# Kernel tuning notes

Measured on AMD Instinct MI355X. Metric: run time of the kernel, lower is better.

## Reference

```python
import jax, jax.numpy as jnp
import numpy as np

N = 50000      # nodes
E = 800000     # edges (avg degree 16)
IN = 128       # input feature dim
HID = 32       # per-head hidden dim
OUT = 64       # per-head output dim
H = 2          # heads per layer
NEG = 0.2      # leaky relu negative slope


def setup_inputs() -> dict:
    key = jax.random.key(0)
    ks = jax.random.split(key, 16)
    x = jax.random.normal(ks[0], (N, IN), dtype=jnp.float32)
    src = jax.random.randint(ks[1], (E,), 0, N)
    dst = jax.random.randint(ks[2], (E,), 0, N)

    def lin(k, fin, fout):
        return jax.random.normal(k, (fin, fout), dtype=jnp.float32) * (1.0 / np.sqrt(fin))

    def attn(k, h, d):
        return jax.random.normal(k, (h, d), dtype=jnp.float32) * 0.1

    # layer 0: IN -> H*HID, layer 1: H*HID -> H*HID, layer 2 (output): H*HID -> H*OUT
    W0, al0, ar0, b0 = lin(ks[3], IN, H * HID), attn(ks[4], H, HID), attn(ks[5], H, HID), jnp.zeros((H * HID,), jnp.float32)
    W1, al1, ar1, b1 = lin(ks[6], H * HID, H * HID), attn(ks[7], H, HID), attn(ks[8], H, HID), jnp.zeros((H * HID,), jnp.float32)
    W2, al2, ar2, b2 = lin(ks[9], H * HID, H * OUT), attn(ks[10], H, OUT), attn(ks[11], H, OUT), jnp.zeros((H * OUT,), jnp.float32)
    return {"x": x, "src": src, "dst": dst,
            "W0": W0, "al0": al0, "ar0": ar0, "b0": b0,
            "W1": W1, "al1": al1, "ar1": ar1, "b1": b1,
            "W2": W2, "al2": al2, "ar2": ar2, "b2": b2}


def gat_conv(x, src, dst, W, al, ar, b, heads, out_dim, apply_relu):
    # feat: [N, H, D]
    feat = (x @ W).reshape(-1, heads, out_dim)
    el = jnp.einsum('nhd,hd->nh', feat, al)   # [N, H]
    er = jnp.einsum('nhd,hd->nh', feat, ar)   # [N, H]
    # per-edge attention logits, leaky-relu
    e = jax.nn.leaky_relu(el[src] + er[dst], NEG)          # [E, H]
    # edge softmax over incoming edges of each dst node (numerically stable)
    m = jax.ops.segment_max(e, dst, num_segments=N)        # [N, H]
    m = jnp.where(jnp.isfinite(m), m, 0.0)                 # nodes w/o in-edges
    ex = jnp.exp(e - m[dst])                               # [E, H]
    s = jax.ops.segment_sum(ex, dst, num_segments=N)       # [N, H]
    alpha = ex / s[dst]                                    # [E, H]
    # weighted aggregate of source features into dst nodes
    rst = jax.ops.segment_sum(feat[src] * alpha[:, :, None], dst, num_segments=N)  # [N, H, D]
    rst = rst + b.reshape(1, heads, out_dim)
    if apply_relu:
        rst = jax.nn.relu(rst)
    return rst


def reference(x, src, dst, W0, al0, ar0, b0, W1, al1, ar1, b1, W2, al2, ar2, b2):
    h = gat_conv(x, src, dst, W0, al0, ar0, b0, H, HID, True).reshape(N, H * HID)   # flatten(1)
    h = gat_conv(h, src, dst, W1, al1, ar1, b1, H, HID, True).reshape(N, H * HID)   # flatten(1)
    logits = gat_conv(h, src, dst, W2, al2, ar2, b2, H, OUT, False).mean(axis=1)    # mean over heads -> [N, OUT]
    return logits
```

## Files before the change

kernel.cpp:

```cpp
#include <hip/hip_runtime.h>
#include <hip/hip_bf16.h>
#include <hip/hip_fp16.h>

#define NNODES 50000
#define NEG_SLOPE 0.2f
#define BKT_SHIFT 8
#define NBKT ((NNODES + 255) >> 8)
#define STRIDE 5120
#define PCHUNK 2048
#define PEPT 8

typedef _Float16 half8 __attribute__((ext_vector_type(8)));
typedef float v4f __attribute__((ext_vector_type(4)));

__device__ __forceinline__ int rfl(int v) { return __builtin_amdgcn_readfirstlane(v); }

__device__ __forceinline__ void pack_one(const float* W, _Float16* Wp, int K, int C, int tid) {
    int KC = K / 32;
    int l = tid & 63;
    int kc = (tid >> 6) % KC;
    int t = tid / (KC * 64);
    int cc = l & 15, q = l >> 4;
    half8 b;
#pragma unroll
    for (int j = 0; j < 8; j++)
        b[j] = (_Float16)W[(size_t)(kc * 32 + q * 8 + j) * C + t * 16 + cc];
    *(half8*)(Wp + (size_t)tid * 8) = b;
}

__global__ __launch_bounds__(256) void kernelAB(
    const float* __restrict__ x, const float* __restrict__ W0,
    const float* __restrict__ AL, const float* __restrict__ AR,
    _Float16* __restrict__ featA, float2* __restrict__ el2A, float2* __restrict__ er2A,
    const float* __restrict__ W2, _Float16* __restrict__ Wp2,
    const int* __restrict__ src, const int* __restrict__ dst,
    int* __restrict__ bcursor, int2* __restrict__ ebuf, int E, int N) {
    int blk = blockIdx.x;
    if (blk >= 786) {
        __shared__ int hist[NBKT];
        __shared__ int gbase[NBKT];
        int t = threadIdx.x;
        for (int i = t; i < NBKT; i += 256) hist[i] = 0;
        __syncthreads();
        int base = (blk - 786) * PCHUNK;
        int sreg[PEPT], dreg[PEPT], rreg[PEPT], breg[PEPT];
#pragma unroll
        for (int k = 0; k < PEPT; k++) {
            int i = base + k * 256 + t;
            if (i < E) {
                sreg[k] = src[i];
                dreg[k] = dst[i];
                breg[k] = dreg[k] >> BKT_SHIFT;
                rreg[k] = atomicAdd(&hist[breg[k]], 1);
            } else {
                breg[k] = -1;
            }
        }
        __syncthreads();
        for (int i = t; i < NBKT; i += 256)
            if (hist[i]) gbase[i] = i * STRIDE + atomicAdd(&bcursor[i * 16], hist[i]);
        __syncthreads();
#pragma unroll
        for (int k = 0; k < PEPT; k++) {
            if (breg[k] >= 0)
                ebuf[(size_t)(gbase[breg[k]] + rreg[k])] = make_int2(sreg[k], dreg[k]);
        }
        return;
    }
    if (blk >= 782) {
        int tid = (blk - 782) * 256 + threadIdx.x;
        if (tid < 8 * 2 * 64) pack_one(W2, Wp2, 64, 128, tid);
        return;
    }
    int wave = threadIdx.x >> 6, lane = threadIdx.x & 63;
    int mtile = blk * 4 + wave;
    if (mtile * 16 >= N) return;
    int m0 = mtile * 16;
    int c = lane & 15, q = lane >> 4;
    v4f acc[4];
#pragma unroll
    for (int t = 0; t < 4; t++) acc[t] = (v4f){0.f, 0.f, 0.f, 0.f};
    const size_t arow = (size_t)(m0 + c) * 128 + q * 8;
#pragma unroll
    for (int kc = 0; kc < 4; kc++) {
        const float* xr = x + arow + kc * 32;
        float4 f0 = *(const float4*)xr;
        float4 f1 = *(const float4*)(xr + 4);
        float fv[8] = {f0.x, f0.y, f0.z, f0.w, f1.x, f1.y, f1.z, f1.w};
        half8 ah, av;
#pragma unroll
        for (int j = 0; j < 8; j++) {
            ah[j] = (_Float16)fv[j];
            av[j] = (_Float16)(fv[j] - (float)ah[j]);
        }
#pragma unroll
        for (int tt = 0; tt < 4; tt++) {
            half8 b;
#pragma unroll
            for (int j = 0; j < 8; j++)
                b[j] = (_Float16)W0[(size_t)(kc * 32 + q * 8 + j) * 64 + tt * 16 + c];
            acc[tt] = __builtin_amdgcn_mfma_f32_16x16x32_f16(ah, b, acc[tt], 0, 0, 0);
            acc[tt] = __builtin_amdgcn_mfma_f32_16x16x32_f16(av, b, acc[tt], 0, 0, 0);
        }
    }
#pragma unroll
    for (int tt = 0; tt < 4; tt++)
#pragma unroll
        for (int r = 0; r < 4; r++) {
            int row = m0 + q * 4 + r;
            featA[(size_t)row * 64 + tt * 16 + c] = (_Float16)acc[tt][r];
        }
    float alv[4], arv[4];
#pragma unroll
    for (int tt = 0; tt < 4; tt++) { alv[tt] = AL[tt * 16 + c]; arv[tt] = AR[tt * 16 + c]; }
#pragma unroll
    for (int r = 0; r < 4; r++) {
        float l0 = 0.f, l1 = 0.f, r0 = 0.f, r1 = 0.f;
#pragma unroll
        for (int tt = 0; tt < 4; tt++) {
            float v = acc[tt][r];
            if (tt < 2) { l0 = fmaf(v, alv[tt], l0); r0 = fmaf(v, arv[tt], r0); }
            else        { l1 = fmaf(v, alv[tt], l1); r1 = fmaf(v, arv[tt], r1); }
        }
#pragma unroll
        for (int m = 1; m < 16; m <<= 1) {
            l0 += __shfl_xor(l0, m, 64);
            l1 += __shfl_xor(l1, m, 64);
            r0 += __shfl_xor(r0, m, 64);
            r1 += __shfl_xor(r1, m, 64);
        }
        if (c == 0) {
            int row = m0 + q * 4 + r;
            el2A[row] = make_float2(l0, l1);
            er2A[row] = make_float2(r0, r1);
        }
    }
}

__global__ __launch_bounds__(1024) void local_sort(const int2* __restrict__ ebuf,
                                                   const int* __restrict__ bcursor,
                                                   int2* __restrict__ rowse,
                                                   int* __restrict__ csrc, int N) {
    __shared__ int lcnt[256], lrow[256], ws[4];
    int b = blockIdx.x;
    int d0 = b << BKT_SHIFT;
    int t = threadIdx.x;
    int base = b * STRIDE;
    int endE = base + bcursor[b * 16];
    if (t < 256) lcnt[t] = 0;
    __syncthreads();
    for (int i = base + t; i < endE; i += 1024)
        atomicAdd(&lcnt[ebuf[i].y - d0], 1);
    __syncthreads();
    int v = (t < 256) ? lcnt[t] : 0;
    int lane = t & 63;
    int x = v;
#pragma unroll
    for (int m = 1; m < 64; m <<= 1) {
        int y = __shfl_up(x, m, 64);
        if (lane >= m) x += y;
    }
    if (t < 256 && lane == 63) ws[t >> 6] = x;
    __syncthreads();
    if (t < 256) {
        int w = t >> 6, waveoff = 0;
#pragma unroll
        for (int k = 0; k < 4; k++) if (k < w) waveoff += ws[k];
        int excl = base + waveoff + x - v;
        lrow[t] = excl;
        int d = d0 + t;
        if (d < N) rowse[d] = make_int2(excl, excl + v);
        lcnt[t] = 0;
    }
    __syncthreads();
    for (int i = base + t; i < endE; i += 1024) {
        int2 e = ebuf[i];
        int ld = e.y - d0;
        int p = lrow[ld] + atomicAdd(&lcnt[ld], 1);
        csrc[p] = e.x;
    }
}

__global__ __launch_bounds__(256) void agg0_gemm1(
    const int2* __restrict__ rowse, const int* __restrict__ csrc,
    const float2* __restrict__ el2A, const float2* __restrict__ er2A,
    const _Float16* __restrict__ featA, const float* __restrict__ b0,
    const float* __restrict__ W1, const float* __restrict__ al1, const float* __restrict__ ar1,
    _Float16* __restrict__ featB, float2* __restrict__ el2B, float2* __restrict__ er2B,
    int N) {
    __shared__ __attribute__((aligned(16))) int   stS[4][64];
    __shared__ __attribute__((aligned(16))) float stX[4][64], stY[4][64];
    __shared__ float vbuf[4][64];
    __shared__ float4 w1v[16 * 64];
    int wave = threadIdx.x >> 6, lane = threadIdx.x & 63, h = lane >> 5;
    for (int i = threadIdx.x; i < 64 * 64; i += 256) {
        int k = i >> 6, cc = i & 63;
        ((float*)w1v)[((((k >> 2) << 6) + cc) << 2) | (k & 3)] = W1[i];
    }
    __syncthreads();
    float bl = b0[lane];
    float al1v = al1[lane], ar1v = ar1[lane];
    const int*   stSw = stS[wave];
    const float* stWH = h ? stY[wave] : stX[wave];
    for (int n0 = blockIdx.x * 4 + wave; n0 < N; n0 += gridDim.x * 4) {
        int n = rfl(n0);
        int2 se = rowse[n];
        int beg = rfl(se.x), end = rfl(se.y);
        float2 rr = er2A[n];
        float s = 0.f, acc = 0.f;
        for (int base = beg; base < end; base += 64) {
            int idx = base + lane;
            bool act = idx < end;
            int sv = act ? csrc[idx] : 0;
            stS[wave][lane] = sv;
            float wxv = 0.f, wyv = 0.f;
            if (act) {
                float2 l = el2A[sv];
                float t0 = l.x + rr.x; t0 = t0 > 0.f ? t0 : NEG_SLOPE * t0;
                float t1 = l.y + rr.y; t1 = t1 > 0.f ? t1 : NEG_SLOPE * t1;
                wxv = __expf(t0); wyv = __expf(t1);
            }
            stX[wave][lane] = wxv;
            stY[wave][lane] = wyv;
            int cnt = (min(64, end - base) + 7) & ~7;
            for (int j = 0; j < cnt; j += 8) {
                int4 sA = *(const int4*)(stSw + j);
                int4 sB = *(const int4*)(stSw + j + 4);
                float f0 = (float)featA[(size_t)sA.x * 64 + lane];
                float f1 = (float)featA[(size_t)sA.y * 64 + lane];
                float f2 = (float)featA[(size_t)sA.z * 64 + lane];
                float f3 = (float)featA[(size_t)sA.w * 64 + lane];
                float f4 = (float)featA[(size_t)sB.x * 64 + lane];
                float f5 = (float)featA[(size_t)sB.y * 64 + lane];
                float f6 = (float)featA[(size_t)sB.z * 64 + lane];
                float f7 = (float)featA[(size_t)sB.w * 64 + lane];
                float4 wv0 = *(const float4*)(stWH + j);
                float4 wv1 = *(const float4*)(stWH + j + 4);
                s += ((wv0.x + wv0.y) + (wv0.z + wv0.w)) + ((wv1.x + wv1.y) + (wv1.z + wv1.w));
                acc = fmaf(wv0.x, f0, acc);
                acc = fmaf(wv0.y, f1, acc);
                acc = fmaf(wv0.z, f2, acc);
                acc = fmaf(wv0.w, f3, acc);
                acc = fmaf(wv1.x, f4, acc);
                acc = fmaf(wv1.y, f5, acc);
                acc = fmaf(wv1.z, f6, acc);
                acc = fmaf(wv1.w, f7, acc);
            }
        }
        float v = (s > 0.f) ? acc / s : 0.f;
        v = fmaxf(v + bl, 0.f);
        vbuf[wave][lane] = v;
        const float4* vv = (const float4*)vbuf[wave];
        float f = 0.f;
#pragma unroll
        for (int kk = 0; kk < 16; kk++) {
            float4 v4 = vv[kk];
            float4 w4 = w1v[(kk << 6) + lane];
            f = fmaf(v4.x, w4.x, f);
            f = fmaf(v4.y, w4.y, f);
            f = fmaf(v4.z, w4.z, f);
            f = fmaf(v4.w, w4.w, f);
        }
        featB[(size_t)n * 64 + lane] = (_Float16)f;
        float vl = f * al1v, vr = f * ar1v;
#pragma unroll
        for (int m = 1; m < 32; m <<= 1) {
            vl += __shfl_xor(vl, m, 64);
            vr += __shfl_xor(vr, m, 64);
        }
        if ((lane & 31) == 0) {
            ((float*)el2B)[n * 2 + h] = vl;
            ((float*)er2B)[n * 2 + h] = vr;
        }
    }
}

__global__ __launch_bounds__(256) void aggregate32(
    const int2* __restrict__ rowse, const int* __restrict__ csrc,
    const float2* __restrict__ el2, const float2* __restrict__ er2,
    const _Float16* __restrict__ feat16, const float* __restrict__ b,
    _Float16* __restrict__ ahi, _Float16* __restrict__ alo, int N) {
    __shared__ __attribute__((aligned(16))) int   stS0[4][64], stS1[4][64];
    __shared__ __attribute__((aligned(16))) float stX0[4][64], stY0[4][64];
    __shared__ __attribute__((aligned(16))) float stX1[4][64], stY1[4][64];
    int wave = threadIdx.x >> 6, lane = threadIdx.x & 63, h = lane >> 5;
    int g = rfl(blockIdx.x * 4 + wave);
    int n0 = 2 * g, n1 = n0 + 1;
    if (n0 >= N) return;
    bool has1 = (n1 < N);
    float bl = b[lane];
    int2 se0 = rowse[n0];
    int2 se1 = has1 ? rowse[n1] : make_int2(0, 0);
    int beg0 = rfl(se0.x), len0 = rfl(se0.y) - beg0;
    int beg1 = rfl(se1.x), len1 = rfl(se1.y) - beg1;
    float2 rr0 = er2[n0];
    float2 rr1 = has1 ? er2[n1] : make_float2(0.f, 0.f);
    const int*   stSw0 = stS0[wave];
    const int*   stSw1 = stS1[wave];
    const float* stWH0 = h ? stY0[wave] : stX0[wave];
    const float* stWH1 = h ? stY1[wave] : stX1[wave];
    float s0 = 0.f, acc0 = 0.f, s1 = 0.f, acc1 = 0.f;
    int chunks = max(len0, len1);
    for (int off = 0; off < chunks; off += 64) {
        bool a0 = off + lane < len0;
        bool a1 = off + lane < len1;
        int sv0 = a0 ? csrc[beg0 + off + lane] : 0;
        int sv1 = a1 ? csrc[beg1 + off + lane] : 0;
        stS0[wave][lane] = sv0;
        stS1[wave][lane] = sv1;
        float wx0 = 0.f, wy0 = 0.f, wx1 = 0.f, wy1 = 0.f;
        if (a0) {
            float2 l = el2[sv0];
            float t0 = l.x + rr0.x; t0 = t0 > 0.f ? t0 : NEG_SLOPE * t0;
            float t1 = l.y + rr0.y; t1 = t1 > 0.f ? t1 : NEG_SLOPE * t1;
            wx0 = __expf(t0); wy0 = __expf(t1);
        }
        if (a1) {
            float2 l = el2[sv1];
            float t0 = l.x + rr1.x; t0 = t0 > 0.f ? t0 : NEG_SLOPE * t0;
            float t1 = l.y + rr1.y; t1 = t1 > 0.f ? t1 : NEG_SLOPE * t1;
            wx1 = __expf(t0); wy1 = __expf(t1);
        }
        stX0[wave][lane] = wx0; stY0[wave][lane] = wy0;
        stX1[wave][lane] = wx1; stY1[wave][lane] = wy1;
        int cnt = (min(64, chunks - off) + 7) & ~7;
        for (int j = 0; j < cnt; j += 8) {
            int4 sA = *(const int4*)(stSw0 + j);
            int4 sB = *(const int4*)(stSw0 + j + 4);
            int4 tA = *(const int4*)(stSw1 + j);
            int4 tB = *(const int4*)(stSw1 + j + 4);
            float f0 = (float)feat16[(size_t)sA.x * 64 + lane];
            float f1 = (float)feat16[(size_t)sA.y * 64 + lane];
            float f2 = (float)feat16[(size_t)sA.z * 64 + lane];
            float f3 = (float)feat16[(size_t)sA.w * 64 + lane];
            float f4 = (float)feat16[(size_t)sB.x * 64 + lane];
            float f5 = (float)feat16[(size_t)sB.y * 64 + lane];
            float f6 = (float)feat16[(size_t)sB.z * 64 + lane];
            float f7 = (float)feat16[(size_t)sB.w * 64 + lane];
            float p0 = (float)feat16[(size_t)tA.x * 64 + lane];
            float p1 = (float)feat16[(size_t)tA.y * 64 + lane];
            float p2 = (float)feat16[(size_t)tA.z * 64 + lane];
            float p3 = (float)feat16[(size_t)tA.w * 64 + lane];
            float p4 = (float)feat16[(size_t)tB.x * 64 + lane];
            float p5 = (float)feat16[(size_t)tB.y * 64 + lane];
            float p6 = (float)feat16[(size_t)tB.z * 64 + lane];
            float p7 = (float)feat16[(size_t)tB.w * 64 + lane];
            float4 wv0 = *(const float4*)(stWH0 + j);
            float4 wv1 = *(const float4*)(stWH0 + j + 4);
            float4 xv0 = *(const float4*)(stWH1 + j);
            float4 xv1 = *(const float4*)(stWH1 + j + 4);
            s0 += ((wv0.x + wv0.y) + (wv0.z + wv0.w)) + ((wv1.x + wv1.y) + (wv1.z + wv1.w));
            acc0 = fmaf(wv0.x, f0, acc0);
            acc0 = fmaf(wv0.y, f1, acc0);
            acc0 = fmaf(wv0.z, f2, acc0);
            acc0 = fmaf(wv0.w, f3, acc0);
            acc0 = fmaf(wv1.x, f4, acc0);
            acc0 = fmaf(wv1.y, f5, acc0);
            acc0 = fmaf(wv1.z, f6, acc0);
            acc0 = fmaf(wv1.w, f7, acc0);
            s1 += ((xv0.x + xv0.y) + (xv0.z + xv0.w)) + ((xv1.x + xv1.y) + (xv1.z + xv1.w));
            acc1 = fmaf(xv0.x, p0, acc1);
            acc1 = fmaf(xv0.y, p1, acc1);
            acc1 = fmaf(xv0.z, p2, acc1);
            acc1 = fmaf(xv0.w, p3, acc1);
            acc1 = fmaf(xv1.x, p4, acc1);
            acc1 = fmaf(xv1.y, p5, acc1);
            acc1 = fmaf(xv1.z, p6, acc1);
            acc1 = fmaf(xv1.w, p7, acc1);
        }
    }
    float v = (s0 > 0.f) ? acc0 / s0 : 0.f;
    v = fmaxf(v + bl, 0.f);
    _Float16 hv = (_Float16)v;
    ahi[(size_t)n0 * 64 + lane] = hv;
    alo[(size_t)n0 * 64 + lane] = (_Float16)(v - (float)hv);
    if (has1) {
        float u = (s1 > 0.f) ? acc1 / s1 : 0.f;
        u = fmaxf(u + bl, 0.f);
        _Float16 hu = (_Float16)u;
        ahi[(size_t)n1 * 64 + lane] = hu;
        alo[(size_t)n1 * 64 + lane] = (_Float16)(u - (float)hu);
    }
}

__global__ __launch_bounds__(256) void gemm_mfma2(
    const _Float16* __restrict__ Ahi, const _Float16* __restrict__ Alo,
    const _Float16* __restrict__ Wp,
    const float* __restrict__ AL, const float* __restrict__ AR,
    __half2* __restrict__ feat2, float2* __restrict__ el2, float2* __restrict__ er2,
    int N) {
    constexpr int KC = 2, NT = 8;
    int wave = threadIdx.x >> 6, lane = threadIdx.x & 63;
    int mtile = blockIdx.x * 4 + wave;
    if (mtile * 16 >= N) return;
    int m0 = mtile * 16;
    int c = lane & 15, q = lane >> 4;
    v4f acc[NT];
#pragma unroll
    for (int t = 0; t < NT; t++) acc[t] = (v4f){0.f, 0.f, 0.f, 0.f};
    const size_t arow = (size_t)(m0 + c) * 64 + q * 8;
#pragma unroll
    for (int kc = 0; kc < KC; kc++) {
        half8 ah = *(const half8*)(Ahi + arow + kc * 32);
        half8 av = *(const half8*)(Alo + arow + kc * 32);
#pragma unroll
        for (int t = 0; t < NT; t++) {
            half8 b = *(const half8*)(Wp + ((size_t)(t * KC + kc) * 64 + lane) * 8);
            acc[t] = __builtin_amdgcn_mfma_f32_16x16x32_f16(ah, b, acc[t], 0, 0, 0);
            acc[t] = __builtin_amdgcn_mfma_f32_16x16x32_f16(av, b, acc[t], 0, 0, 0);
        }
    }
#pragma unroll
    for (int t = 0; t < NT / 2; t++)
#pragma unroll
        for (int r = 0; r < 4; r++) {
            int row = m0 + q * 4 + r;
            feat2[(size_t)row * 64 + t * 16 + c] =
                __floats2half2_rn(acc[t][r], acc[t + NT / 2][r]);
        }
    float alv[NT], arv[NT];
#pragma unroll
    for (int t = 0; t < NT; t++) { alv[t] = AL[t * 16 + c]; arv[t] = AR[t * 16 + c]; }
#pragma unroll
    for (int r = 0; r < 4; r++) {
        float l0 = 0.f, l1 = 0.f, r0 = 0.f, r1 = 0.f;
#pragma unroll
        for (int t = 0; t < NT; t++) {
            float v = acc[t][r];
            if (t < NT / 2) { l0 = fmaf(v, alv[t], l0); r0 = fmaf(v, arv[t], r0); }
            else            { l1 = fmaf(v, alv[t], l1); r1 = fmaf(v, arv[t], r1); }
        }
#pragma unroll
        for (int m = 1; m < 16; m <<= 1) {
            l0 += __shfl_xor(l0, m, 64);
            l1 += __shfl_xor(l1, m, 64);
            r0 += __shfl_xor(r0, m, 64);
            r1 += __shfl_xor(r1, m, 64);
        }
        if (c == 0) {
            int row = m0 + q * 4 + r;
            el2[row] = make_float2(l0, l1);
            er2[row] = make_float2(r0, r1);
        }
    }
}

__global__ __launch_bounds__(256) void aggregate64_mean(
    const int2* __restrict__ rowse, const int* __restrict__ csrc,
    const float2* __restrict__ el2, const float2* __restrict__ er2,
    const __half2* __restrict__ feat2, const float* __restrict__ b,
    float* __restrict__ out, int N) {
    __shared__ __attribute__((aligned(16))) int   stS0[4][64], stS1[4][64];
    __shared__ __attribute__((aligned(16))) float stX0[4][64], stY0[4][64];
    __shared__ __attribute__((aligned(16))) float stX1[4][64], stY1[4][64];
    int wave = threadIdx.x >> 6, lane = threadIdx.x & 63;
    int g = rfl(blockIdx.x * 4 + wave);
    int n0 = 2 * g, n1 = n0 + 1;
    if (n0 >= N) return;
    bool has1 = (n1 < N);
    float b0v = b[lane], b1v = b[64 + lane];
    int2 se0 = rowse[n0];
    int2 se1 = has1 ? rowse[n1] : make_int2(0, 0);
    int beg0 = rfl(se0.x), len0 = rfl(se0.y) - beg0;
    int beg1 = rfl(se1.x), len1 = rfl(se1.y) - beg1;
    float2 rr0 = er2[n0];
    float2 rr1 = has1 ? er2[n1] : make_float2(0.f, 0.f);
    const int* stSw0 = stS0[wave];
    const int* stSw1 = stS1[wave];
    float s00 = 0.f, s01 = 0.f, a00 = 0.f, a01 = 0.f;
    float s10 = 0.f, s11 = 0.f, a10 = 0.f, a11 = 0.f;
    int chunks = max(len0, len1);
    for (int off = 0; off < chunks; off += 64) {
        bool a0 = off + lane < len0;
        bool a1 = off + lane < len1;
        int sv0 = a0 ? csrc[beg0 + off + lane] : 0;
        int sv1 = a1 ? csrc[beg1 + off + lane] : 0;
        stS0[wave][lane] = sv0;
        stS1[wave][lane] = sv1;
        float wx0 = 0.f, wy0 = 0.f, wx1 = 0.f, wy1 = 0.f;
        if (a0) {
            float2 l = el2[sv0];
            float t0 = l.x + rr0.x; t0 = t0 > 0.f ? t0 : NEG_SLOPE * t0;
            float t1 = l.y + rr0.y; t1 = t1 > 0.f ? t1 : NEG_SLOPE * t1;
            wx0 = __expf(t0); wy0 = __expf(t1);
        }
        if (a1) {
            float2 l = el2[sv1];
            float t0 = l.x + rr1.x; t0 = t0 > 0.f ? t0 : NEG_SLOPE * t0;
            float t1 = l.y + rr1.y; t1 = t1 > 0.f ? t1 : NEG_SLOPE * t1;
            wx1 = __expf(t0); wy1 = __expf(t1);
        }
        stX0[wave][lane] = wx0; stY0[wave][lane] = wy0;
        stX1[wave][lane] = wx1; stY1[wave][lane] = wy1;
        int cnt = (min(64, chunks - off) + 7) & ~7;
        for (int j = 0; j < cnt; j += 8) {
            int4 sA = *(const int4*)(stSw0 + j);
            int4 sB = *(const int4*)(stSw0 + j + 4);
            int4 tA = *(const int4*)(stSw1 + j);
            int4 tB = *(const int4*)(stSw1 + j + 4);
            float2 fv0[8], fv1[8];
            fv0[0] = __half22float2(feat2[(size_t)sA.x * 64 + lane]);
            fv0[1] = __half22float2(feat2[(size_t)sA.y * 64 + lane]);
            fv0[2] = __half22float2(feat2[(size_t)sA.z * 64 + lane]);
            fv0[3] = __half22float2(feat2[(size_t)sA.w * 64 + lane]);
            fv0[4] = __half22float2(feat2[(size_t)sB.x * 64 + lane]);
            fv0[5] = __half22float2(feat2[(size_t)sB.y * 64 + lane]);
            fv0[6] = __half22float2(feat2[(size_t)sB.z * 64 + lane]);
            fv0[7] = __half22float2(feat2[(size_t)sB.w * 64 + lane]);
            fv1[0] = __half22float2(feat2[(size_t)tA.x * 64 + lane]);
            fv1[1] = __half22float2(feat2[(size_t)tA.y * 64 + lane]);
            fv1[2] = __half22float2(feat2[(size_t)tA.z * 64 + lane]);
            fv1[3] = __half22float2(feat2[(size_t)tA.w * 64 + lane]);
            fv1[4] = __half22float2(feat2[(size_t)tB.x * 64 + lane]);
            fv1[5] = __half22float2(feat2[(size_t)tB.y * 64 + lane]);
            fv1[6] = __half22float2(feat2[(size_t)tB.z * 64 + lane]);
            fv1[7] = __half22float2(feat2[(size_t)tB.w * 64 + lane]);
            float4 wx0v = *(const float4*)(stX0[wave] + j);
            float4 wx0w = *(const float4*)(stX0[wave] + j + 4);
            float4 wy0v = *(const float4*)(stY0[wave] + j);
            float4 wy0w = *(const float4*)(stY0[wave] + j + 4);
            float4 wx1v = *(const float4*)(stX1[wave] + j);
            float4 wx1w = *(const float4*)(stX1[wave] + j + 4);
            float4 wy1v = *(const float4*)(stY1[wave] + j);
            float4 wy1w = *(const float4*)(stY1[wave] + j + 4);
            float wxs0[8] = {wx0v.x, wx0v.y, wx0v.z, wx0v.w, wx0w.x, wx0w.y, wx0w.z, wx0w.w};
            float wys0[8] = {wy0v.x, wy0v.y, wy0v.z, wy0v.w, wy0w.x, wy0w.y, wy0w.z, wy0w.w};
            float wxs1[8] = {wx1v.x, wx1v.y, wx1v.z, wx1v.w, wx1w.x, wx1w.y, wx1w.z, wx1w.w};
            float wys1[8] = {wy1v.x, wy1v.y, wy1v.z, wy1v.w, wy1w.x, wy1w.y, wy1w.z, wy1w.w};
#pragma unroll
            for (int u = 0; u < 8; u++) {
                s00 += wxs0[u]; s01 += wys0[u];
                a00 = fmaf(wxs0[u], fv0[u].x, a00);
                a01 = fmaf(wys0[u], fv0[u].y, a01);
            }
#pragma unroll
            for (int u = 0; u < 8; u++) {
                s10 += wxs1[u]; s11 += wys1[u];
                a10 = fmaf(wxs1[u], fv1[u].x, a10);
                a11 = fmaf(wys1[u], fv1[u].y, a11);
            }
        }
    }
    float v0 = (s00 > 0.f) ? a00 / s00 : 0.f;
    float v1 = (s01 > 0.f) ? a01 / s01 : 0.f;
    out[(size_t)n0 * 64 + lane] = 0.5f * ((v0 + b0v) + (v1 + b1v));
    if (has1) {
        float u0 = (s10 > 0.f) ? a10 / s10 : 0.f;
        float u1 = (s11 > 0.f) ? a11 / s11 : 0.f;
        out[(size_t)n1 * 64 + lane] = 0.5f * ((u0 + b0v) + (u1 + b1v));
    }
}


extern "C" void kernel_launch(void* const* d_in, const int* in_sizes, int n_in,
                              void* d_out, int out_size, void* d_ws, size_t ws_size,
                              hipStream_t stream) {
    const float* x   = (const float*)d_in[0];
    const int*   src = (const int*)d_in[1];
    const int*   dst = (const int*)d_in[2];
    const float* W0  = (const float*)d_in[3];
    const float* al0 = (const float*)d_in[4];
    const float* ar0 = (const float*)d_in[5];
    const float* b0  = (const float*)d_in[6];
    const float* W1  = (const float*)d_in[7];
    const float* al1 = (const float*)d_in[8];
    const float* ar1 = (const float*)d_in[9];
    const float* b1  = (const float*)d_in[10];
    const float* W2  = (const float*)d_in[11];
    const float* al2 = (const float*)d_in[12];
    const float* ar2 = (const float*)d_in[13];
    const float* b2  = (const float*)d_in[14];
    float* out = (float*)d_out;

    const int N = NNODES;
    const int E = in_sizes[1];

    char* p = (char*)d_ws;
    auto alloc = [&](size_t bytes) {
        void* r = (void*)p;
        p += (bytes + 255) & ~(size_t)255;
        return r;
    };
    int*    bcursor = (int*)alloc((size_t)NBKT * 16 * 4);
    int2*   rowse   = (int2*)alloc((size_t)N * 8);
    int2*   ebuf    = (int2*)alloc(((size_t)NBKT * STRIDE + 4096) * 8);
    int*    csrc    = (int*)alloc(((size_t)NBKT * STRIDE + 4096) * 4);
    float2* el2A    = (float2*)alloc((size_t)N * 8);
    float2* er2A    = (float2*)alloc((size_t)N * 8);
    float2* el2B    = (float2*)alloc((size_t)N * 8);
    float2* er2B    = (float2*)alloc((size_t)N * 8);
    _Float16* ahi   = (_Float16*)alloc((size_t)N * 64 * 2);
    _Float16* alo   = (_Float16*)alloc((size_t)N * 64 * 2);
    void*   featA   = alloc((size_t)N * 64 * 4);
    _Float16* featB = (_Float16*)alloc((size_t)N * 64 * 2);
    _Float16* Wp2   = (_Float16*)alloc(8 * 2 * 64 * 8 * 2);

    hipMemsetAsync(bcursor, 0, (size_t)NBKT * 16 * 4, stream);
    int nch = (E + PCHUNK - 1) / PCHUNK;
    kernelAB<<<786 + nch, 256, 0, stream>>>(x, W0, al0, ar0, (_Float16*)featA, el2A, er2A,
                                            W2, Wp2, src, dst, bcursor, ebuf, E, N);
    local_sort<<<NBKT, 1024, 0, stream>>>(ebuf, bcursor, rowse, csrc, N);

    agg0_gemm1<<<2048, 256, 0, stream>>>(rowse, csrc, el2A, er2A, (const _Float16*)featA,
                                         b0, W1, al1, ar1, featB, el2B, er2B, N);
    int npair = (N + 1) / 2;
    int nbp = (npair + 3) / 4;
    aggregate32<<<nbp, 256, 0, stream>>>(rowse, csrc, el2B, er2B, featB, b1, ahi, alo, N);
    int gb = (N / 16 + 3) / 4;
    gemm_mfma2<<<gb, 256, 0, stream>>>(ahi, alo, Wp2, al2, ar2, (__half2*)featA, el2A, er2A, N);
    aggregate64_mean<<<nbp, 256, 0, stream>>>(rowse, csrc, el2A, er2A, (const __half2*)featA,
                                              b2, out, N);
}
```

Measured before the change: 225.0 us.

## Regroup launches: partition with weight packing, then co-schedule local sort with GEMM0

```diff
diff --git a/kernel.cpp b/kernel.cpp
--- a/kernel.cpp
+++ b/kernel.cpp
@@ -28,52 +28,101 @@
     *(half8*)(Wp + (size_t)tid * 8) = b;
 }
 
-__global__ __launch_bounds__(256) void kernelAB(
-    const float* __restrict__ x, const float* __restrict__ W0,
+__global__ __launch_bounds__(256) void kernelP(
+    const int* __restrict__ src, const int* __restrict__ dst,
+    int* __restrict__ bcursor, int2* __restrict__ ebuf,
+    const float* __restrict__ W0, _Float16* __restrict__ Wp0,
+    const float* __restrict__ W2, _Float16* __restrict__ Wp2,
+    int E, int nch) {
+    int blk = blockIdx.x;
+    if (blk >= nch + 4) {
+        int tid = (blk - nch - 4) * 256 + threadIdx.x;
+        if (tid < 8 * 2 * 64) pack_one(W2, Wp2, 64, 128, tid);
+        return;
+    }
+    if (blk >= nch) {
+        int tid = (blk - nch) * 256 + threadIdx.x;
+        if (tid < 4 * 4 * 64) pack_one(W0, Wp0, 128, 64, tid);
+        return;
+    }
+    __shared__ int hist[NBKT];
+    __shared__ int gbase[NBKT];
+    int t = threadIdx.x;
+    for (int i = t; i < NBKT; i += 256) hist[i] = 0;
+    __syncthreads();
+    int base = blk * PCHUNK;
+    int sreg[PEPT], dreg[PEPT], rreg[PEPT], breg[PEPT];
+#pragma unroll
+    for (int k = 0; k < PEPT; k++) {
+        int i = base + k * 256 + t;
+        if (i < E) {
+            sreg[k] = src[i];
+            dreg[k] = dst[i];
+            breg[k] = dreg[k] >> BKT_SHIFT;
+            rreg[k] = atomicAdd(&hist[breg[k]], 1);
+        } else {
+            breg[k] = -1;
+        }
+    }
+    __syncthreads();
+    for (int i = t; i < NBKT; i += 256)
+        if (hist[i]) gbase[i] = i * STRIDE + atomicAdd(&bcursor[i * 16], hist[i]);
+    __syncthreads();
+#pragma unroll
+    for (int k = 0; k < PEPT; k++) {
+        if (breg[k] >= 0)
+            ebuf[(size_t)(gbase[breg[k]] + rreg[k])] = make_int2(sreg[k], dreg[k]);
+    }
+}
+
+__global__ __launch_bounds__(256) void kernelAB2(
+    const float* __restrict__ x, const _Float16* __restrict__ Wp0,
     const float* __restrict__ AL, const float* __restrict__ AR,
     _Float16* __restrict__ featA, float2* __restrict__ el2A, float2* __restrict__ er2A,
-    const float* __restrict__ W2, _Float16* __restrict__ Wp2,
-    const int* __restrict__ src, const int* __restrict__ dst,
-    int* __restrict__ bcursor, int2* __restrict__ ebuf, int E, int N) {
+    const int2* __restrict__ ebuf, const int* __restrict__ bcursor,
+    int2* __restrict__ rowse, int* __restrict__ csrc, int N) {
     int blk = blockIdx.x;
-    if (blk >= 786) {
-        __shared__ int hist[NBKT];
-        __shared__ int gbase[NBKT];
+    if (blk < NBKT) {
+        __shared__ int lcnt[256], lrow[256], ws[4];
+        int b = blk;
+        int d0 = b << BKT_SHIFT;
         int t = threadIdx.x;
-        for (int i = t; i < NBKT; i += 256) hist[i] = 0;
+        int base = b * STRIDE;
+        int endE = base + bcursor[b * 16];
+        lcnt[t] = 0;
         __syncthreads();
-        int base = (blk - 786) * PCHUNK;
-        int sreg[PEPT], dreg[PEPT], rreg[PEPT], breg[PEPT];
-#pragma unroll
-        for (int k = 0; k < PEPT; k++) {
-            int i = base + k * 256 + t;
-            if (i < E) {
-                sreg[k] = src[i];
-                dreg[k] = dst[i];
-                breg[k] = dreg[k] >> BKT_SHIFT;
-                rreg[k] = atomicAdd(&hist[breg[k]], 1);
-            } else {
-                breg[k] = -1;
-            }
-        }
+        for (int i = base + t; i < endE; i += 256)
+            atomicAdd(&lcnt[ebuf[i].y - d0], 1);
         __syncthreads();
-        for (int i = t; i < NBKT; i += 256)
-            if (hist[i]) gbase[i] = i * STRIDE + atomicAdd(&bcursor[i * 16], hist[i]);
+        int v = lcnt[t];
+        int lane = t & 63;
+        int xx = v;
+#pragma unroll
+        for (int m = 1; m < 64; m <<= 1) {
+            int y = __shfl_up(xx, m, 64);
+            if (lane >= m) xx += y;
+        }
+        if (lane == 63) ws[t >> 6] = xx;
         __syncthreads();
-#pragma unroll
-        for (int k = 0; k < PEPT; k++) {
-            if (breg[k] >= 0)
-                ebuf[(size_t)(gbase[breg[k]] + rreg[k])] = make_int2(sreg[k], dreg[k]);
+        int w = t >> 6, waveoff = 0;
+#pragma unroll
+        for (int k = 0; k < 4; k++) if (k < w) waveoff += ws[k];
+        int excl = base + waveoff + xx - v;
+        lrow[t] = excl;
+        int d = d0 + t;
+        if (d < N) rowse[d] = make_int2(excl, excl + v);
+        lcnt[t] = 0;
+        __syncthreads();
+        for (int i = base + t; i < endE; i += 256) {
+            int2 e = ebuf[i];
+            int ld = e.y - d0;
+            int p = lrow[ld] + atomicAdd(&lcnt[ld], 1);
+            csrc[p] = e.x;
         }
         return;
     }
-    if (blk >= 782) {
-        int tid = (blk - 782) * 256 + threadIdx.x;
-        if (tid < 8 * 2 * 64) pack_one(W2, Wp2, 64, 128, tid);
-        return;
-    }
     int wave = threadIdx.x >> 6, lane = threadIdx.x & 63;
-    int mtile = blk * 4 + wave;
+    int mtile = (blk - NBKT) * 4 + wave;
     if (mtile * 16 >= N) return;
     int m0 = mtile * 16;
     int c = lane & 15, q = lane >> 4;
@@ -95,10 +144,7 @@
         }
 #pragma unroll
         for (int tt = 0; tt < 4; tt++) {
-            half8 b;
-#pragma unroll
-            for (int j = 0; j < 8; j++)
-                b[j] = (_Float16)W0[(size_t)(kc * 32 + q * 8 + j) * 64 + tt * 16 + c];
+            half8 b = *(const half8*)(Wp0 + ((size_t)(tt * 4 + kc) * 64 + lane) * 8);
             acc[tt] = __builtin_amdgcn_mfma_f32_16x16x32_f16(ah, b, acc[tt], 0, 0, 0);
             acc[tt] = __builtin_amdgcn_mfma_f32_16x16x32_f16(av, b, acc[tt], 0, 0, 0);
         }
@@ -134,50 +180,6 @@
             el2A[row] = make_float2(l0, l1);
             er2A[row] = make_float2(r0, r1);
         }
-    }
-}
-
-__global__ __launch_bounds__(1024) void local_sort(const int2* __restrict__ ebuf,
-                                                   const int* __restrict__ bcursor,
-                                                   int2* __restrict__ rowse,
-                                                   int* __restrict__ csrc, int N) {
-    __shared__ int lcnt[256], lrow[256], ws[4];
-    int b = blockIdx.x;
-    int d0 = b << BKT_SHIFT;
-    int t = threadIdx.x;
-    int base = b * STRIDE;
-    int endE = base + bcursor[b * 16];
-    if (t < 256) lcnt[t] = 0;
-    __syncthreads();
-    for (int i = base + t; i < endE; i += 1024)
-        atomicAdd(&lcnt[ebuf[i].y - d0], 1);
-    __syncthreads();
-    int v = (t < 256) ? lcnt[t] : 0;
-    int lane = t & 63;
-    int x = v;
-#pragma unroll
-    for (int m = 1; m < 64; m <<= 1) {
-        int y = __shfl_up(x, m, 64);
-        if (lane >= m) x += y;
-    }
-    if (t < 256 && lane == 63) ws[t >> 6] = x;
-    __syncthreads();
-    if (t < 256) {
-        int w = t >> 6, waveoff = 0;
-#pragma unroll
-        for (int k = 0; k < 4; k++) if (k < w) waveoff += ws[k];
-        int excl = base + waveoff + x - v;
-        lrow[t] = excl;
-        int d = d0 + t;
-        if (d < N) rowse[d] = make_int2(excl, excl + v);
-        lcnt[t] = 0;
-    }
-    __syncthreads();
-    for (int i = base + t; i < endE; i += 1024) {
-        int2 e = ebuf[i];
-        int ld = e.y - d0;
-        int p = lrow[ld] + atomicAdd(&lcnt[ld], 1);
-        csrc[p] = e.x;
     }
 }
 
@@ -594,13 +596,13 @@
     void*   featA   = alloc((size_t)N * 64 * 4);
     _Float16* featB = (_Float16*)alloc((size_t)N * 64 * 2);
     _Float16* Wp2   = (_Float16*)alloc(8 * 2 * 64 * 8 * 2);
+    _Float16* Wp0   = (_Float16*)alloc(4 * 4 * 64 * 8 * 2);
 
     hipMemsetAsync(bcursor, 0, (size_t)NBKT * 16 * 4, stream);
     int nch = (E + PCHUNK - 1) / PCHUNK;
-    kernelAB<<<786 + nch, 256, 0, stream>>>(x, W0, al0, ar0, (_Float16*)featA, el2A, er2A,
-                                            W2, Wp2, src, dst, bcursor, ebuf, E, N);
-    local_sort<<<NBKT, 1024, 0, stream>>>(ebuf, bcursor, rowse, csrc, N);
-
+    kernelP<<<nch + 8, 256, 0, stream>>>(src, dst, bcursor, ebuf, W0, Wp0, W2, Wp2, E, nch);
+    kernelAB2<<<NBKT + 782, 256, 0, stream>>>(x, Wp0, al0, ar0, (_Float16*)featA, el2A, er2A,
+                                              ebuf, bcursor, rowse, csrc, N);
     agg0_gemm1<<<2048, 256, 0, stream>>>(rowse, csrc, el2A, er2A, (const _Float16*)featA,
                                          b0, W1, al1, ar1, featB, el2B, er2B, N);
     int npair = (N + 1) / 2;
```

New measurement: 230.6 us. 2.5% more time.

## Split layer-1 fused aggregate+FMA GEMM into aggregate32 plus MFMA GEMM kernel

Applied to the files above, without the earlier changes.

```diff
diff --git a/kernel.cpp b/kernel.cpp
--- a/kernel.cpp
+++ b/kernel.cpp
@@ -33,16 +33,17 @@
     const float* __restrict__ AL, const float* __restrict__ AR,
     _Float16* __restrict__ featA, float2* __restrict__ el2A, float2* __restrict__ er2A,
     const float* __restrict__ W2, _Float16* __restrict__ Wp2,
+    const float* __restrict__ W1, _Float16* __restrict__ Wp1,
     const int* __restrict__ src, const int* __restrict__ dst,
     int* __restrict__ bcursor, int2* __restrict__ ebuf, int E, int N) {
     int blk = blockIdx.x;
-    if (blk >= 786) {
+    if (blk >= 788) {
         __shared__ int hist[NBKT];
         __shared__ int gbase[NBKT];
         int t = threadIdx.x;
         for (int i = t; i < NBKT; i += 256) hist[i] = 0;
         __syncthreads();
-        int base = (blk - 786) * PCHUNK;
+        int base = (blk - 788) * PCHUNK;
         int sreg[PEPT], dreg[PEPT], rreg[PEPT], breg[PEPT];
 #pragma unroll
         for (int k = 0; k < PEPT; k++) {
@@ -65,6 +66,11 @@
             if (breg[k] >= 0)
                 ebuf[(size_t)(gbase[breg[k]] + rreg[k])] = make_int2(sreg[k], dreg[k]);
         }
+        return;
+    }
+    if (blk >= 786) {
+        int tid = (blk - 786) * 256 + threadIdx.x;
+        if (tid < 4 * 2 * 64) pack_one(W1, Wp1, 64, 64, tid);
         return;
     }
     if (blk >= 782) {
@@ -178,100 +184,6 @@
         int ld = e.y - d0;
         int p = lrow[ld] + atomicAdd(&lcnt[ld], 1);
         csrc[p] = e.x;
-    }
-}
-
-__global__ __launch_bounds__(256) void agg0_gemm1(
-    const int2* __restrict__ rowse, const int* __restrict__ csrc,
-    const float2* __restrict__ el2A, const float2* __restrict__ er2A,
-    const _Float16* __restrict__ featA, const float* __restrict__ b0,
-    const float* __restrict__ W1, const float* __restrict__ al1, const float* __restrict__ ar1,
-    _Float16* __restrict__ featB, float2* __restrict__ el2B, float2* __restrict__ er2B,
-    int N) {
-    __shared__ __attribute__((aligned(16))) int   stS[4][64];
-    __shared__ __attribute__((aligned(16))) float stX[4][64], stY[4][64];
-    __shared__ float vbuf[4][64];
-    __shared__ float4 w1v[16 * 64];
-    int wave = threadIdx.x >> 6, lane = threadIdx.x & 63, h = lane >> 5;
-    for (int i = threadIdx.x; i < 64 * 64; i += 256) {
-        int k = i >> 6, cc = i & 63;
-        ((float*)w1v)[((((k >> 2) << 6) + cc) << 2) | (k & 3)] = W1[i];
-    }
-    __syncthreads();
-    float bl = b0[lane];
-    float al1v = al1[lane], ar1v = ar1[lane];
-    const int*   stSw = stS[wave];
-    const float* stWH = h ? stY[wave] : stX[wave];
-    for (int n0 = blockIdx.x * 4 + wave; n0 < N; n0 += gridDim.x * 4) {
-        int n = rfl(n0);
-        int2 se = rowse[n];
-        int beg = rfl(se.x), end = rfl(se.y);
-        float2 rr = er2A[n];
-        float s = 0.f, acc = 0.f;
-        for (int base = beg; base < end; base += 64) {
-            int idx = base + lane;
-            bool act = idx < end;
-            int sv = act ? csrc[idx] : 0;
-            stS[wave][lane] = sv;
-            float wxv = 0.f, wyv = 0.f;
-            if (act) {
-                float2 l = el2A[sv];
-                float t0 = l.x + rr.x; t0 = t0 > 0.f ? t0 : NEG_SLOPE * t0;
-                float t1 = l.y + rr.y; t1 = t1 > 0.f ? t1 : NEG_SLOPE * t1;
-                wxv = __expf(t0); wyv = __expf(t1);
-            }
-            stX[wave][lane] = wxv;
-            stY[wave][lane] = wyv;
-            int cnt = (min(64, end - base) + 7) & ~7;
-            for (int j = 0; j < cnt; j += 8) {
-                int4 sA = *(const int4*)(stSw + j);
-                int4 sB = *(const int4*)(stSw + j + 4);
-                float f0 = (float)featA[(size_t)sA.x * 64 + lane];
-                float f1 = (float)featA[(size_t)sA.y * 64 + lane];
-                float f2 = (float)featA[(size_t)sA.z * 64 + lane];
-                float f3 = (float)featA[(size_t)sA.w * 64 + lane];
-                float f4 = (float)featA[(size_t)sB.x * 64 + lane];
-                float f5 = (float)featA[(size_t)sB.y * 64 + lane];
-                float f6 = (float)featA[(size_t)sB.z * 64 + lane];
-                float f7 = (float)featA[(size_t)sB.w * 64 + lane];
-                float4 wv0 = *(const float4*)(stWH + j);
-                float4 wv1 = *(const float4*)(stWH + j + 4);
-                s += ((wv0.x + wv0.y) + (wv0.z + wv0.w)) + ((wv1.x + wv1.y) + (wv1.z + wv1.w));
-                acc = fmaf(wv0.x, f0, acc);
-                acc = fmaf(wv0.y, f1, acc);
-                acc = fmaf(wv0.z, f2, acc);
-                acc = fmaf(wv0.w, f3, acc);
-                acc = fmaf(wv1.x, f4, acc);
-                acc = fmaf(wv1.y, f5, acc);
-                acc = fmaf(wv1.z, f6, acc);
-                acc = fmaf(wv1.w, f7, acc);
-            }
-        }
-        float v = (s > 0.f) ? acc / s : 0.f;
-        v = fmaxf(v + bl, 0.f);
-        vbuf[wave][lane] = v;
-        const float4* vv = (const float4*)vbuf[wave];
-        float f = 0.f;
-#pragma unroll
-        for (int kk = 0; kk < 16; kk++) {
-            float4 v4 = vv[kk];
-            float4 w4 = w1v[(kk << 6) + lane];
-            f = fmaf(v4.x, w4.x, f);
-            f = fmaf(v4.y, w4.y, f);
-            f = fmaf(v4.z, w4.z, f);
-            f = fmaf(v4.w, w4.w, f);
-        }
-        featB[(size_t)n * 64 + lane] = (_Float16)f;
-        float vl = f * al1v, vr = f * ar1v;
-#pragma unroll
-        for (int m = 1; m < 32; m <<= 1) {
-            vl += __shfl_xor(vl, m, 64);
-            vr += __shfl_xor(vr, m, 64);
-        }
-        if ((lane & 31) == 0) {
-            ((float*)el2B)[n * 2 + h] = vl;
-            ((float*)er2B)[n * 2 + h] = vr;
-        }
     }
 }
 
@@ -383,6 +295,67 @@
     }
 }
 
+__global__ __launch_bounds__(256) void gemm_mfma1(
+    const _Float16* __restrict__ Ahi, const _Float16* __restrict__ Alo,
+    const _Float16* __restrict__ Wp,
+    const float* __restrict__ AL, const float* __restrict__ AR,
+    _Float16* __restrict__ featB, float2* __restrict__ el2, float2* __restrict__ er2,
+    int N) {
+    constexpr int KC = 2, NT = 4;
+    int wave = threadIdx.x >> 6, lane = threadIdx.x & 63;
+    int mtile = blockIdx.x * 4 + wave;
+    if (mtile * 16 >= N) return;
+    int m0 = mtile * 16;
+    int c = lane & 15, q = lane >> 4;
+    v4f acc[NT];
+#pragma unroll
+    for (int t = 0; t < NT; t++) acc[t] = (v4f){0.f, 0.f, 0.f, 0.f};
+    const size_t arow = (size_t)(m0 + c) * 64 + q * 8;
+#pragma unroll
+    for (int kc = 0; kc < KC; kc++) {
+        half8 ah = *(const half8*)(Ahi + arow + kc * 32);
+        half8 av = *(const half8*)(Alo + arow + kc * 32);
+#pragma unroll
+        for (int t = 0; t < NT; t++) {
+            half8 b = *(const half8*)(Wp + ((size_t)(t * KC + kc) * 64 + lane) * 8);
+            acc[t] = __builtin_amdgcn_mfma_f32_16x16x32_f16(ah, b, acc[t], 0, 0, 0);
+            acc[t] = __builtin_amdgcn_mfma_f32_16x16x32_f16(av, b, acc[t], 0, 0, 0);
+        }
+    }
+#pragma unroll
+    for (int t = 0; t < NT; t++)
+#pragma unroll
+        for (int r = 0; r < 4; r++) {
+            int row = m0 + q * 4 + r;
+            featB[(size_t)row * 64 + t * 16 + c] = (_Float16)acc[t][r];
+        }
+    float alv[NT], arv[NT];
+#pragma unroll
+    for (int t = 0; t < NT; t++) { alv[t] = AL[t * 16 + c]; arv[t] = AR[t * 16 + c]; }
+#pragma unroll
+    for (int r = 0; r < 4; r++) {
+        float l0 = 0.f, l1 = 0.f, r0 = 0.f, r1 = 0.f;
+#pragma unroll
+        for (int t = 0; t < NT; t++) {
+            float v = acc[t][r];
+            if (t < 2) { l0 = fmaf(v, alv[t], l0); r0 = fmaf(v, arv[t], r0); }
+            else       { l1 = fmaf(v, alv[t], l1); r1 = fmaf(v, arv[t], r1); }
+        }
+#pragma unroll
+        for (int m = 1; m < 16; m <<= 1) {
+            l0 += __shfl_xor(l0, m, 64);
+            l1 += __shfl_xor(l1, m, 64);
+            r0 += __shfl_xor(r0, m, 64);
+            r1 += __shfl_xor(r1, m, 64);
+        }
+        if (c == 0) {
+            int row = m0 + q * 4 + r;
+            el2[row] = make_float2(l0, l1);
+            er2[row] = make_float2(r0, r1);
+        }
+    }
+}
+
 __global__ __launch_bounds__(256) void gemm_mfma2(
     const _Float16* __restrict__ Ahi, const _Float16* __restrict__ Alo,
     const _Float16* __restrict__ Wp,
@@ -591,22 +564,26 @@
     float2* er2B    = (float2*)alloc((size_t)N * 8);
     _Float16* ahi   = (_Float16*)alloc((size_t)N * 64 * 2);
     _Float16* alo   = (_Float16*)alloc((size_t)N * 64 * 2);
+    _Float16* vhi0  = (_Float16*)alloc((size_t)N * 64 * 2);
+    _Float16* vlo0  = (_Float16*)alloc((size_t)N * 64 * 2);
     void*   featA   = alloc((size_t)N * 64 * 4);
     _Float16* featB = (_Float16*)alloc((size_t)N * 64 * 2);
     _Float16* Wp2   = (_Float16*)alloc(8 * 2 * 64 * 8 * 2);
+    _Float16* Wp1   = (_Float16*)alloc(4 * 2 * 64 * 8 * 2);
 
     hipMemsetAsync(bcursor, 0, (size_t)NBKT * 16 * 4, stream);
     int nch = (E + PCHUNK - 1) / PCHUNK;
-    kernelAB<<<786 + nch, 256, 0, stream>>>(x, W0, al0, ar0, (_Float16*)featA, el2A, er2A,
-                                            W2, Wp2, src, dst, bcursor, ebuf, E, N);
+    kernelAB<<<788 + nch, 256, 0, stream>>>(x, W0, al0, ar0, (_Float16*)featA, el2A, er2A,
+                                            W2, Wp2, W1, Wp1, src, dst, bcursor, ebuf, E, N);
     local_sort<<<NBKT, 1024, 0, stream>>>(ebuf, bcursor, rowse, csrc, N);
 
-    agg0_gemm1<<<2048, 256, 0, stream>>>(rowse, csrc, el2A, er2A, (const _Float16*)featA,
-                                         b0, W1, al1, ar1, featB, el2B, er2B, N);
     int npair = (N + 1) / 2;
     int nbp = (npair + 3) / 4;
+    int gb = (N / 16 + 3) / 4;
+    aggregate32<<<nbp, 256, 0, stream>>>(rowse, csrc, el2A, er2A, (const _Float16*)featA,
+                                         b0, vhi0, vlo0, N);
+    gemm_mfma1<<<gb, 256, 0, stream>>>(vhi0, vlo0, Wp1, al1, ar1, featB, el2B, er2B, N);
     aggregate32<<<nbp, 256, 0, stream>>>(rowse, csrc, el2B, er2B, featB, b1, ahi, alo, N);
-    int gb = (N / 16 + 3) / 4;
     gemm_mfma2<<<gb, 256, 0, stream>>>(ahi, alo, Wp2, al2, ar2, (__half2*)featA, el2A, er2A, N);
     aggregate64_mean<<<nbp, 256, 0, stream>>>(rowse, csrc, el2A, er2A, (const __half2*)featA,
                                               b2, out, N);
```

New measurement: 213.2 us. 5.3% less time.
